# Performance work log

Measured on AMD Instinct MI355X. Metric: run time of the kernel, lower is better.

The kernel has to match this reference:

```python
import jax, jax.numpy as jnp
import numpy as np

HEADS = 8
HEAD_DIM = 32
DIM = 256        # embed_dim; inner_dim = HEADS*HEAD_DIM = 256
DEPTH = 2
MLP_DIM = 1024
GRID_H, GRID_W = 64, 64
CELL_DIM = 15    # pe(0) + in(3) + out(3) + hidden(9)
PE_IN = 3        # cell_pe_patch_dim + cell_in_patch_dim
UPDATE_DIM = 12  # cell_out(3) + hidden(9)
BATCH = 8


def layer_norm(x, g, b, eps=1e-5):
    m = jnp.mean(x, axis=-1, keepdims=True)
    v = jnp.var(x, axis=-1, keepdims=True)
    return (x - m) * jax.lax.rsqrt(v + eps) * g + b


def vit_positional_encoding(n, dim):
    pos = jnp.arange(n, dtype=jnp.float32)[:, None]
    div = jnp.exp(jnp.arange(0, dim, 2, dtype=jnp.float32) * (-np.log(10000.0) / dim))
    pe = jnp.zeros((n, dim), dtype=jnp.float32)
    pe = pe.at[:, 0::2].set(jnp.sin(pos * div)).at[:, 1::2].set(jnp.cos(pos * div))
    return pe[None]  # [1, n, dim]


def localize(x, H, W):
    # x: [b, heads, n, d] with n = H*W. Gather circular 3x3 neighbourhood per position
    # (equivalent to circular pad + one-hot conv in the torch LocalizeAttention).
    b, nh, n, d = x.shape
    y = x.reshape(b, nh, H, W, d)
    neigh = [jnp.roll(y, (1 - ki, 1 - kj), axis=(2, 3)) for ki in range(3) for kj in range(3)]
    return jnp.stack(neigh, axis=4).reshape(b, nh, n, 9, d)  # [b, h, n, 9, d]


def setup_inputs() -> dict:
    key = jax.random.key(0)
    ks = jax.random.split(key, 20)
    d = {}
    d['cells'] = jax.random.normal(ks[0], (BATCH, CELL_DIM, GRID_H, GRID_W), dtype=jnp.float32)
    s = 0.02
    d['We'] = jax.random.normal(ks[1], (CELL_DIM, DIM), jnp.float32) * s
    d['be'] = jnp.zeros((DIM,), jnp.float32)
    d['ln1_g'] = jnp.ones((DEPTH, DIM), jnp.float32)
    d['ln1_b'] = jnp.zeros((DEPTH, DIM), jnp.float32)
    d['Wqkv'] = jax.random.normal(ks[2], (DEPTH, DIM, 3 * HEADS * HEAD_DIM), jnp.float32) * s
    d['Wo'] = jax.random.normal(ks[3], (DEPTH, HEADS * HEAD_DIM, DIM), jnp.float32) * s
    d['bo'] = jnp.zeros((DEPTH, DIM), jnp.float32)
    d['ln2_g'] = jnp.ones((DEPTH, DIM), jnp.float32)
    d['ln2_b'] = jnp.zeros((DEPTH, DIM), jnp.float32)
    d['W1'] = jax.random.normal(ks[4], (DEPTH, DIM, MLP_DIM), jnp.float32) * s
    d['b1'] = jnp.zeros((DEPTH, MLP_DIM), jnp.float32)
    d['W2'] = jax.random.normal(ks[5], (DEPTH, MLP_DIM, DIM), jnp.float32) * s
    d['b2'] = jnp.zeros((DEPTH, DIM), jnp.float32)
    d['lnh_g'] = jnp.ones((DIM,), jnp.float32)
    d['lnh_b'] = jnp.zeros((DIM,), jnp.float32)
    # NOTE: torch zero-inits mlp_head; we use small random weights so the output is nontrivial.
    d['Wh'] = jax.random.normal(ks[6], (DIM, UPDATE_DIM), jnp.float32) * s
    d['bh'] = jnp.zeros((UPDATE_DIM,), jnp.float32)
    return d


def reference(cells, We, be, ln1_g, ln1_b, Wqkv, Wo, bo, ln2_g, ln2_b,
              W1, b1, W2, b2, lnh_g, lnh_b, Wh, bh):
    b, c, H, W = cells.shape
    n = H * W
    x = cells.reshape(b, c, n).transpose(0, 2, 1)           # b n c
    x = x @ We + be                                         # cell_to_embedding
    x = x + vit_positional_encoding(n, x.shape[-1])
    scale = HEAD_DIM ** -0.5
    for l in range(DEPTH):
        y = layer_norm(x, ln1_g[l], ln1_b[l])
        qkv = y @ Wqkv[l]                                   # b n 3*inner
        q, k, v = jnp.split(qkv, 3, axis=-1)
        split_heads = lambda t: t.reshape(b, n, HEADS, HEAD_DIM).transpose(0, 2, 1, 3)
        q, k, v = split_heads(q), split_heads(k), split_heads(v)  # b h n d
        kl = localize(k, H, W)                              # b h n 9 d
        vl = localize(v, H, W)
        dots = jnp.einsum('bhnd,bhnkd->bhnk', q, kl) * scale
        attn = jax.nn.softmax(dots, axis=-1)
        out = jnp.einsum('bhnk,bhnkd->bhnd', attn, vl)
        out = out.transpose(0, 2, 1, 3).reshape(b, n, HEADS * HEAD_DIM)
        x = out @ Wo[l] + bo[l] + x                         # attention + residual
        y = layer_norm(x, ln2_g[l], ln2_b[l])
        y = jax.nn.gelu(y @ W1[l] + b1[l], approximate=False) @ W2[l] + b2[l]
        x = x + y                                           # ffn + residual
    upd = layer_norm(x, lnh_g, lnh_b) @ Wh + bh             # b n UPDATE_DIM
    upd = upd.transpose(0, 2, 1).reshape(b, UPDATE_DIM, H, W)
    # update_rate = 1.0 -> deterministic branch: cells[:, PE_IN:] + update
    updated = cells[:, PE_IN:] + upd
    return jnp.concatenate([cells[:, :PE_IN], updated], axis=1)
```

## Files before the change

### kernel.cpp

```cpp
#include <hip/hip_runtime.h>
#include <hip/hip_bf16.h>
#include <math.h>

#define HEADS 8
#define HEAD_DIM 32
#define DIM 256
#define MLP_DIM 1024
#define NTOK 4096
#define BATCH 8
#define M_TOK (BATCH*NTOK)
#define CELL_DIM 15
#define PE_IN 3
#define UPD 12
#define HME ((size_t)M_TOK*32)

typedef __attribute__((ext_vector_type(8))) short bf16x8;
typedef __attribute__((ext_vector_type(4))) float f32x4;

static __device__ __forceinline__ float bf2f(unsigned short u) {
    return __uint_as_float(((unsigned int)u) << 16);
}
static __device__ __forceinline__ unsigned short f2bf(float f) {
    __hip_bfloat16 h = __float2bfloat16(f);
    union { __hip_bfloat16 h; unsigned short u; } cv; cv.h = h; return cv.u;
}
static __device__ __forceinline__ void gload_lds16(const unsigned short* g, unsigned short* l) {
    __builtin_amdgcn_global_load_lds(
        (const __attribute__((address_space(1))) void*)g,
        (__attribute__((address_space(3))) void*)l, 16, 0, 0);
}
static __device__ __forceinline__ float gelu_fast(float v) {
    return v / (1.f + __expf(-1.59576912f * (v + 0.044715f * v * v * v)));
}

__global__ __launch_bounds__(256) void k_embed(const float* __restrict__ cells,
        const float* __restrict__ We, const float* __restrict__ be,
        const float* __restrict__ g, const float* __restrict__ bln,
        unsigned short* __restrict__ x, unsigned short* __restrict__ y) {
    __shared__ float red[8];
    int tok = blockIdx.x;
    int d = threadIdx.x;
    int b = tok >> 12, n = tok & 4095;
    const float* cb = cells + (size_t)b * CELL_DIM * NTOK + n;
    float acc = 0.f;
#pragma unroll
    for (int c = 0; c < CELL_DIM; ++c)
        acc += cb[c * NTOK] * We[c * DIM + d];
    int i = d >> 1;
    float freq = __expf(-0.03597789f * (float)(2 * i));
    float ph = (float)n * freq;
    float pe = (d & 1) ? __cosf(ph) : __sinf(ph);
    float v = acc + be[d] + pe;
    x[(size_t)tok * DIM + d] = f2bf(v);
    float s = v, ss = v * v;
#pragma unroll
    for (int off = 32; off; off >>= 1) { s += __shfl_xor(s, off); ss += __shfl_xor(ss, off); }
    int wave = d >> 6, lane = d & 63;
    if (lane == 0) { red[wave] = s; red[4 + wave] = ss; }
    __syncthreads();
    float stot = red[0] + red[1] + red[2] + red[3];
    float sstot = red[4] + red[5] + red[6] + red[7];
    float mean = stot * (1.f / DIM);
    float rstd = rsqrtf(sstot * (1.f / DIM) - mean * mean + 1e-5f);
    y[(size_t)tok * DIM + d] = f2bf((v - mean) * rstd * g[d] + bln[d]);
}

__global__ __launch_bounds__(256) void k_prep(const float* __restrict__ Wqkv,
        const float* __restrict__ Wo, const float* __restrict__ W1,
        const float* __restrict__ W2, const float* __restrict__ Wh,
        unsigned short* __restrict__ wT) {
    int seg = blockIdx.y;
    int idx = blockIdx.x * 256 + threadIdx.x;
    if (seg == 8) {
        if (idx >= 16 * 256) return;
        int u = idx >> 8, k = idx & 255;
        wT[1572864 + idx] = (u < UPD) ? f2bf(Wh[(size_t)k * UPD + u]) : (unsigned short)0;
        return;
    }
    int l = seg >> 2, mat = seg & 3;
    const float* src; int kwSh, Nw; size_t ooff;
    switch (mat) {
        case 0: src = Wqkv + (size_t)l * 196608; kwSh = 8;  Nw = 768;  ooff = (size_t)l * 786432 + 0;      break;
        case 1: src = Wo   + (size_t)l * 65536;  kwSh = 8;  Nw = 256;  ooff = (size_t)l * 786432 + 196608; break;
        case 2: src = W1   + (size_t)l * 262144; kwSh = 8;  Nw = 1024; ooff = (size_t)l * 786432 + 262144; break;
        default:src = W2   + (size_t)l * 262144; kwSh = 10; Nw = 256;  ooff = (size_t)l * 786432 + 524288; break;
    }
    int Kw = 1 << kwSh;
    if (idx >= Kw * Nw) return;
    int n = idx >> kwSh, k = idx & (Kw - 1);
    wT[ooff + idx] = f2bf(src[(size_t)k * Nw + n]);
}

template<int EPI, int KT>
__global__ __launch_bounds__(512, 4) void k_mgemm(const unsigned short* __restrict__ A,
        const unsigned short* __restrict__ BT, const float* __restrict__ bias,
        void* __restrict__ Cout, int M, int N, int NT) {
    __shared__ unsigned short As[4][128 * 32];
    __shared__ unsigned short Bs[4][128 * 32];
    int bid = blockIdx.x;
    int cpx = gridDim.x >> 3;
    int sb = (bid & 7) * cpx + (bid >> 3);
    int mt = sb / NT, nt = sb - mt * NT;
    int m0 = mt * 128, n0 = nt * 128;
    int t = threadIdx.x;
    int lane = t & 63, w = t >> 6;
    int wm = (w >> 2) * 64, wn = (w & 3) * 32;
    f32x4 acc[4][2] = {};
    int srow = t >> 2;
    int cg = (t & 3) ^ ((srow >> 1) & 3);
    const unsigned short* aBase = A  + (size_t)(m0 + srow) * KT + cg * 8;
    const unsigned short* bBase = BT + (size_t)(n0 + srow) * KT + cg * 8;
    int fr = lane & 15, kb8 = lane >> 4;

    auto stage = [&](int buf, int k0) {
        gload_lds16(aBase + k0, &As[0][0] + buf * 4096 + t * 8);
        gload_lds16(bBase + k0, &Bs[0][0] + buf * 4096 + t * 8);
    };
    auto compute = [&](int buf) {
        const unsigned short* a = &As[0][0] + buf * 4096;
        const unsigned short* b = &Bs[0][0] + buf * 4096;
        bf16x8 af[4], bfv[2];
#pragma unroll
        for (int i = 0; i < 4; ++i) {
            int r_ = wm + i * 16 + fr;
            af[i] = *(const bf16x8*)&a[r_ * 32 + ((kb8 ^ ((r_ >> 1) & 3)) << 3)];
        }
#pragma unroll
        for (int j = 0; j < 2; ++j) {
            int r_ = wn + j * 16 + fr;
            bfv[j] = *(const bf16x8*)&b[r_ * 32 + ((kb8 ^ ((r_ >> 1) & 3)) << 3)];
        }
        __builtin_amdgcn_s_setprio(1);
#pragma unroll
        for (int i = 0; i < 4; ++i)
#pragma unroll
            for (int j = 0; j < 2; ++j)
                acc[i][j] = __builtin_amdgcn_mfma_f32_16x16x32_bf16(bfv[j], af[i], acc[i][j], 0, 0, 0);
        __builtin_amdgcn_s_setprio(0);
    };

    constexpr int NK = KT >> 5;
    stage(0, 0);
    stage(1, 32);
    stage(2, 64);
    asm volatile("s_waitcnt vmcnt(4)" ::: "memory");
    __builtin_amdgcn_s_barrier();
    __builtin_amdgcn_sched_barrier(0);
#pragma unroll
    for (int k = 0; k < NK - 1; ++k) {
        if (k + 3 < NK) stage((k + 3) & 3, (k + 3) * 32);
        compute(k & 3);
        __builtin_amdgcn_sched_barrier(0);
        if (k + 3 < NK)      asm volatile("s_waitcnt vmcnt(4)" ::: "memory");
        else if (k + 2 < NK) asm volatile("s_waitcnt vmcnt(2)" ::: "memory");
        else                 asm volatile("s_waitcnt vmcnt(0)" ::: "memory");
        __builtin_amdgcn_s_barrier();
        __builtin_amdgcn_sched_barrier(0);
    }
    compute((NK - 1) & 3);

    int mcol = lane & 15, nq = (lane >> 4) * 4;
#pragma unroll
    for (int i = 0; i < 4; ++i) {
        int m = m0 + wm + i * 16 + mcol;
#pragma unroll
        for (int j = 0; j < 2; ++j) {
            int ng = n0 + wn + j * 16 + nq;
            if (EPI == 3) {
                int type = ng >> 8, rem = ng & 255;
                ushort4 pk;
                pk.x = f2bf(acc[i][j][0]); pk.y = f2bf(acc[i][j][1]);
                pk.z = f2bf(acc[i][j][2]); pk.w = f2bf(acc[i][j][3]);
                *(ushort4*)((unsigned short*)Cout +
                    (size_t)(type * 8 + (rem >> 5)) * HME + (size_t)m * 32 + (rem & 31)) = pk;
            } else {
                float4 b4 = *(const float4*)&bias[ng];
                ushort4 pk;
                pk.x = f2bf(gelu_fast(acc[i][j][0] + b4.x));
                pk.y = f2bf(gelu_fast(acc[i][j][1] + b4.y));
                pk.z = f2bf(gelu_fast(acc[i][j][2] + b4.z));
                pk.w = f2bf(gelu_fast(acc[i][j][3] + b4.w));
                *(ushort4*)((unsigned short*)Cout + (size_t)m * N + ng) = pk;
            }
        }
    }
}

template<int ALAYOUT>
__global__ __launch_bounds__(512, 4) void k_mgemm_ln(const unsigned short* __restrict__ A,
        const unsigned short* __restrict__ BT, const float* __restrict__ bias,
        const float* __restrict__ g, const float* __restrict__ bln,
        unsigned short* __restrict__ x, unsigned short* __restrict__ y, int K) {
    __shared__ unsigned short As[3][64 * 32];
    __shared__ unsigned short Bs[3][256 * 32];
    float* sred = (float*)&As[0][0];
    float* ssred = sred + 512;
    float* msr = ssred + 512;
    int t = threadIdx.x;
    int lane = t & 63, w = t >> 6;
    int wn = w * 32;
    int m0 = blockIdx.x * 64;
    int mloc = lane & 15, nq = (lane >> 4) * 4;

    ushort4 xres[4][2];
#pragma unroll
    for (int i = 0; i < 4; ++i) {
        int gm = m0 + i * 16 + mloc;
#pragma unroll
        for (int j = 0; j < 2; ++j)
            xres[i][j] = *(const ushort4*)&x[(size_t)gm * DIM + wn + j * 16 + nq];
    }
    __builtin_amdgcn_sched_barrier(0);

    f32x4 acc[4][2] = {};
    int rB0 = t >> 2, cgB0 = (t & 3) ^ ((rB0 >> 1) & 3);
    int c1 = t + 512;
    int rB1 = c1 >> 2, cgB1 = (c1 & 3) ^ ((rB1 >> 1) & 3);
    int tA = t & 255;
    int rA = tA >> 2, cgA = (tA & 3) ^ ((rA >> 1) & 3);
    const unsigned short* aBase = (ALAYOUT == 0)
        ? A + (size_t)(m0 + rA) * K + cgA * 8
        : A + (size_t)(m0 + rA) * 32 + cgA * 8;
    const unsigned short* b0Base = BT + (size_t)rB0 * K + cgB0 * 8;
    const unsigned short* b1Base = BT + (size_t)rB1 * K + cgB1 * 8;
    int fr = lane & 15, kb8 = lane >> 4;

    auto stage = [&](int buf, int k0) {
        unsigned short* as_ = &As[0][0] + buf * 2048;
        unsigned short* bs_ = &Bs[0][0] + buf * 8192;
        gload_lds16(b0Base + k0, bs_ + t * 8);
        gload_lds16(b1Base + k0, bs_ + 4096 + t * 8);
        if (t < 256) {
            const unsigned short* aSrc = (ALAYOUT == 0) ? aBase + k0 : aBase + (size_t)(k0 >> 5) * HME;
            gload_lds16(aSrc, as_ + tA * 8);
        } else {
            gload_lds16(b0Base + k0, bs_ + t * 8);
        }
    };
    auto compute = [&](int buf) {
        const unsigned short* as_ = &As[0][0] + buf * 2048;
        const unsigned short* bs_ = &Bs[0][0] + buf * 8192;
        bf16x8 af[4], bfv[2];
#pragma unroll
        for (int i = 0; i < 4; ++i) {
            int r_ = i * 16 + fr;
            af[i] = *(const bf16x8*)&as_[r_ * 32 + ((kb8 ^ ((r_ >> 1) & 3)) << 3)];
        }
#pragma unroll
        for (int j = 0; j < 2; ++j) {
            int rl = wn + j * 16 + fr;
            bfv[j] = *(const bf16x8*)&bs_[rl * 32 + ((kb8 ^ ((rl >> 1) & 3)) << 3)];
        }
        __builtin_amdgcn_s_setprio(1);
#pragma unroll
        for (int i = 0; i < 4; ++i)
#pragma unroll
            for (int j = 0; j < 2; ++j)
                acc[i][j] = __builtin_amdgcn_mfma_f32_16x16x32_bf16(bfv[j], af[i], acc[i][j], 0, 0, 0);
        __builtin_amdgcn_s_setprio(0);
    };

    int nk = K >> 5;
    stage(0, 0);
    stage(1, 32);
    asm volatile("s_waitcnt vmcnt(3)" ::: "memory");
    __builtin_amdgcn_s_barrier();
    __builtin_amdgcn_sched_barrier(0);
    int cur = 0;
    for (int k = 0; k < nk - 1; ++k) {
        int pre = k + 2;
        if (pre < nk) {
            int preBuf = cur + 2; if (preBuf >= 3) preBuf -= 3;
            stage(preBuf, pre * 32);
        }
        compute(cur);
        __builtin_amdgcn_sched_barrier(0);
        if (pre < nk) asm volatile("s_waitcnt vmcnt(3)" ::: "memory");
        else          asm volatile("s_waitcnt vmcnt(0)" ::: "memory");
        __builtin_amdgcn_s_barrier();
        __builtin_amdgcn_sched_barrier(0);
        ++cur; if (cur >= 3) cur -= 3;
    }
    compute(cur);
    __syncthreads();

#pragma unroll
    for (int i = 0; i < 4; ++i) {
        float s = 0.f, ss = 0.f;
#pragma unroll
        for (int j = 0; j < 2; ++j) {
            int nb = wn + j * 16 + nq;
            float4 b4 = *(const float4*)&bias[nb];
            acc[i][j][0] += b4.x + bf2f(xres[i][j].x);
            acc[i][j][1] += b4.y + bf2f(xres[i][j].y);
            acc[i][j][2] += b4.z + bf2f(xres[i][j].z);
            acc[i][j][3] += b4.w + bf2f(xres[i][j].w);
#pragma unroll
            for (int r = 0; r < 4; ++r) { float v = acc[i][j][r]; s += v; ss += v * v; }
        }
        s += __shfl_xor(s, 16); ss += __shfl_xor(ss, 16);
        s += __shfl_xor(s, 32); ss += __shfl_xor(ss, 32);
        if (lane < 16) {
            int row = i * 16 + lane;
            sred[row * 8 + w] = s;
            ssred[row * 8 + w] = ss;
        }
    }
    __syncthreads();
    if (t < 64) {
        float s = 0.f, ss = 0.f;
#pragma unroll
        for (int q = 0; q < 8; ++q) { s += sred[t * 8 + q]; ss += ssred[t * 8 + q]; }
        float mean = s * (1.f / DIM);
        float var = ss * (1.f / DIM) - mean * mean;
        msr[t * 2] = mean;
        msr[t * 2 + 1] = rsqrtf(var + 1e-5f);
    }
    __syncthreads();
#pragma unroll
    for (int i = 0; i < 4; ++i) {
        int row = i * 16 + mloc;
        int gm = m0 + row;
        float mean = msr[row * 2], rstd = msr[row * 2 + 1];
#pragma unroll
        for (int j = 0; j < 2; ++j) {
            int nb = wn + j * 16 + nq;
            float4 gv4 = *(const float4*)&g[nb];
            float4 bb4 = *(const float4*)&bln[nb];
            ushort4 xo;
            xo.x = f2bf(acc[i][j][0]); xo.y = f2bf(acc[i][j][1]);
            xo.z = f2bf(acc[i][j][2]); xo.w = f2bf(acc[i][j][3]);
            *(ushort4*)&x[(size_t)gm * DIM + nb] = xo;
            ushort4 yv;
            yv.x = f2bf((acc[i][j][0] - mean) * rstd * gv4.x + bb4.x);
            yv.y = f2bf((acc[i][j][1] - mean) * rstd * gv4.y + bb4.y);
            yv.z = f2bf((acc[i][j][2] - mean) * rstd * gv4.z + bb4.z);
            yv.w = f2bf((acc[i][j][3] - mean) * rstd * gv4.w + bb4.w);
            *(ushort4*)&y[(size_t)gm * DIM + nb] = yv;
        }
    }
}

__global__ __launch_bounds__(256) void k_attn(const unsigned short* __restrict__ qkvH,
        unsigned short* __restrict__ attnH) {
    int t = threadIdx.x;
    int h = t >> 5, tl = t & 31;
    int tok = blockIdx.x * 32 + tl;
    int b = tok >> 12, n = tok & 4095;
    int r = n >> 6, c = n & 63;

    float q[32];
    {
        const uint4* u = (const uint4*)(qkvH + (size_t)h * HME + (size_t)tok * 32);
#pragma unroll
        for (int i = 0; i < 4; ++i) {
            uint4 x4 = u[i];
            unsigned wv[4] = {x4.x, x4.y, x4.z, x4.w};
#pragma unroll
            for (int wj = 0; wj < 4; ++wj) {
                q[i * 8 + wj * 2]     = __uint_as_float(wv[wj] << 16);
                q[i * 8 + wj * 2 + 1] = __uint_as_float(wv[wj] & 0xffff0000u);
            }
        }
    }
    int nts[9];
    float dots[9];
    const unsigned short* kbase = qkvH + (size_t)(8 + h) * HME;
#pragma unroll
    for (int ki = 0; ki < 3; ++ki)
#pragma unroll
        for (int kj = 0; kj < 3; ++kj) {
            int rr = (r + ki - 1) & 63, cc = (c + kj - 1) & 63;
            int nt = (b << 12) + (rr << 6) + cc;
            nts[ki * 3 + kj] = nt;
            const uint4* u = (const uint4*)(kbase + (size_t)nt * 32);
            float acc = 0.f;
#pragma unroll
            for (int i = 0; i < 4; ++i) {
                uint4 x4 = u[i];
                unsigned wv[4] = {x4.x, x4.y, x4.z, x4.w};
#pragma unroll
                for (int wj = 0; wj < 4; ++wj) {
                    acc += __uint_as_float(wv[wj] << 16)        * q[i * 8 + wj * 2];
                    acc += __uint_as_float(wv[wj] & 0xffff0000u) * q[i * 8 + wj * 2 + 1];
                }
            }
            dots[ki * 3 + kj] = acc * 0.17677669529f;
        }
    float m = dots[0];
#pragma unroll
    for (int j = 1; j < 9; ++j) m = fmaxf(m, dots[j]);
    float sum = 0.f;
#pragma unroll
    for (int j = 0; j < 9; ++j) { dots[j] = __expf(dots[j] - m); sum += dots[j]; }
    float inv = 1.f / sum;
    float o[32] = {};
    const unsigned short* vbase = qkvH + (size_t)(16 + h) * HME;
#pragma unroll
    for (int j = 0; j < 9; ++j) {
        float wgt = dots[j] * inv;
        const uint4* u = (const uint4*)(vbase + (size_t)nts[j] * 32);
#pragma unroll
        for (int i = 0; i < 4; ++i) {
            uint4 x4 = u[i];
            unsigned wv[4] = {x4.x, x4.y, x4.z, x4.w};
#pragma unroll
            for (int wj = 0; wj < 4; ++wj) {
                o[i * 8 + wj * 2]     += wgt * __uint_as_float(wv[wj] << 16);
                o[i * 8 + wj * 2 + 1] += wgt * __uint_as_float(wv[wj] & 0xffff0000u);
            }
        }
    }
    uint4 st[4];
    unsigned* sw = (unsigned*)st;
#pragma unroll
    for (int i = 0; i < 16; ++i)
        sw[i] = (unsigned)f2bf(o[2 * i]) | ((unsigned)f2bf(o[2 * i + 1]) << 16);
    uint4* od = (uint4*)(attnH + (size_t)h * HME + (size_t)tok * 32);
#pragma unroll
    for (int i = 0; i < 4; ++i) od[i] = st[i];
}

__global__ __launch_bounds__(256) void k_headgemv(const unsigned short* __restrict__ y,
        const unsigned short* __restrict__ WhT, float* __restrict__ Cg) {
    int t = threadIdx.x, lane = t & 63, w = t >> 6;
    int m0 = blockIdx.x * 64 + w * 16;
    int fr = lane & 15, kb = (lane >> 4) * 8;
    f32x4 acc = {};
    const unsigned short* aRow = y + (size_t)(m0 + fr) * DIM + kb;
    const unsigned short* bRow = WhT + (size_t)fr * DIM + kb;
#pragma unroll
    for (int k0 = 0; k0 < DIM; k0 += 32) {
        bf16x8 a = *(const bf16x8*)(aRow + k0);
        bf16x8 bfr = *(const bf16x8*)(bRow + k0);
        acc = __builtin_amdgcn_mfma_f32_16x16x32_bf16(a, bfr, acc, 0, 0, 0);
    }
    int col = lane & 15, rowq = (lane >> 4) * 4;
#pragma unroll
    for (int r = 0; r < 4; ++r)
        Cg[(size_t)(m0 + rowq + r) * 16 + col] = acc[r];
}

__global__ __launch_bounds__(256) void k_assemble(const float* __restrict__ cells,
        const float* __restrict__ Cg, const float* __restrict__ bh,
        float* __restrict__ outp) {
    int idx = blockIdx.x * 256 + threadIdx.x;
    int total = BATCH * CELL_DIM * (NTOK / 4);
    if (idx >= total) return;
    int n4 = idx & 1023;
    int c = (idx >> 10) % CELL_DIM;
    int b = idx / (CELL_DIM * 1024);
    size_t ci = ((size_t)b * CELL_DIM + c) * NTOK + n4 * 4;
    float4 o = *(const float4*)(cells + ci);
    if (c >= PE_IN) {
        int u = c - PE_IN;
        float bias = bh[u];
        size_t tok = (size_t)b * NTOK + n4 * 4;
        o.x += Cg[(tok + 0) * 16 + u] + bias;
        o.y += Cg[(tok + 1) * 16 + u] + bias;
        o.z += Cg[(tok + 2) * 16 + u] + bias;
        o.w += Cg[(tok + 3) * 16 + u] + bias;
    }
    *(float4*)(outp + ci) = o;
}

extern "C" void kernel_launch(void* const* d_in, const int* in_sizes, int n_in,
                              void* d_out, int out_size, void* d_ws, size_t ws_size,
                              hipStream_t stream) {
    const float* cells = (const float*)d_in[0];
    const float* We    = (const float*)d_in[1];
    const float* be    = (const float*)d_in[2];
    const float* ln1_g = (const float*)d_in[3];
    const float* ln1_b = (const float*)d_in[4];
    const float* Wqkv  = (const float*)d_in[5];
    const float* Wo    = (const float*)d_in[6];
    const float* bo    = (const float*)d_in[7];
    const float* ln2_g = (const float*)d_in[8];
    const float* ln2_b = (const float*)d_in[9];
    const float* W1    = (const float*)d_in[10];
    const float* b1    = (const float*)d_in[11];
    const float* W2    = (const float*)d_in[12];
    const float* b2    = (const float*)d_in[13];
    const float* lnh_g = (const float*)d_in[14];
    const float* lnh_b = (const float*)d_in[15];
    const float* Wh    = (const float*)d_in[16];
    const float* bh    = (const float*)d_in[17];
    float* outp = (float*)d_out;

    char* ws = (char*)d_ws;
    unsigned short* x = (unsigned short*)ws;
    unsigned short* y = (unsigned short*)(ws + 33554432);
    unsigned short* scratch = (unsigned short*)(ws + 50331648);
    unsigned short* wT = (unsigned short*)(ws + 117440512);
    unsigned short* qkvH  = scratch;
    unsigned short* attnH = scratch + 24 * HME;
    unsigned short* hidden = scratch;
    float* Cg = (float*)scratch;

    k_prep<<<dim3(1024, 9), 256, 0, stream>>>(Wqkv, Wo, W1, W2, Wh, wT);
    k_embed<<<M_TOK, 256, 0, stream>>>(cells, We, be, ln1_g, ln1_b, x, y);
    for (int l = 0; l < 2; ++l) {
        const unsigned short* wL = wT + (size_t)l * 786432;
        const float* gN = (l == 0) ? ln1_g + DIM : lnh_g;
        const float* bN = (l == 0) ? ln1_b + DIM : lnh_b;
        k_mgemm<3, 256><<<1536, 512, 0, stream>>>(
            y, wL + 0, nullptr, qkvH, M_TOK, 768, 6);
        k_attn<<<M_TOK / 32, 256, 0, stream>>>(qkvH, attnH);
        k_mgemm_ln<1><<<M_TOK / 64, 512, 0, stream>>>(
            attnH, wL + 196608, bo + l * DIM, ln2_g + l * DIM, ln2_b + l * DIM, x, y, DIM);
        k_mgemm<1, 256><<<2048, 512, 0, stream>>>(
            y, wL + 262144, b1 + l * MLP_DIM, hidden, M_TOK, MLP_DIM, 8);
        k_mgemm_ln<0><<<M_TOK / 64, 512, 0, stream>>>(
            hidden, wL + 524288, b2 + l * DIM, gN, bN, x, y, MLP_DIM);
    }
    k_headgemv<<<M_TOK / 64, 256, 0, stream>>>(y, wT + 1572864, Cg);
    k_assemble<<<(BATCH * CELL_DIM * (NTOK / 4) + 255) / 256, 256, 0, stream>>>(cells, Cg, bh, outp);
}
```

Baseline: 368.2 us.

## Make QKV and FFN1 GEMMs persistent over four M-tiles with continuous pipeline

```diff
diff --git a/kernel.cpp b/kernel.cpp
--- a/kernel.cpp
+++ b/kernel.cpp
@@ -91,7 +91,7 @@
     wT[ooff + idx] = f2bf(src[(size_t)k * Nw + n]);
 }
 
-template<int EPI, int KT>
+template<int EPI, int KT, int T>
 __global__ __launch_bounds__(512, 4) void k_mgemm(const unsigned short* __restrict__ A,
         const unsigned short* __restrict__ BT, const float* __restrict__ bias,
         void* __restrict__ Cout, int M, int N, int NT) {
@@ -100,21 +100,26 @@
     int bid = blockIdx.x;
     int cpx = gridDim.x >> 3;
     int sb = (bid & 7) * cpx + (bid >> 3);
-    int mt = sb / NT, nt = sb - mt * NT;
-    int m0 = mt * 128, n0 = nt * 128;
+    int mg = sb / NT, nt = sb - mg * NT;
+    int m0g = mg * (128 * T), n0 = nt * 128;
     int t = threadIdx.x;
     int lane = t & 63, w = t >> 6;
     int wm = (w >> 2) * 64, wn = (w & 3) * 32;
     f32x4 acc[4][2] = {};
     int srow = t >> 2;
     int cg = (t & 3) ^ ((srow >> 1) & 3);
-    const unsigned short* aBase = A  + (size_t)(m0 + srow) * KT + cg * 8;
+    const unsigned short* aBase = A  + (size_t)(m0g + srow) * KT + cg * 8;
     const unsigned short* bBase = BT + (size_t)(n0 + srow) * KT + cg * 8;
     int fr = lane & 15, kb8 = lane >> 4;
-
-    auto stage = [&](int buf, int k0) {
-        gload_lds16(aBase + k0, &As[0][0] + buf * 4096 + t * 8);
-        gload_lds16(bBase + k0, &Bs[0][0] + buf * 4096 + t * 8);
+    constexpr int NK = KT >> 5;
+    constexpr int S = NK * T;
+
+    auto stageU = [&](int u) {
+        int buf = u & 3;
+        int tau = u >> 3, kk = u & 7;
+        gload_lds16(aBase + (size_t)tau * 128 * KT + kk * 32,
+                    &As[0][0] + buf * 4096 + t * 8);
+        gload_lds16(bBase + kk * 32, &Bs[0][0] + buf * 4096 + t * 8);
     };
     auto compute = [&](int buf) {
         const unsigned short* a = &As[0][0] + buf * 4096;
@@ -138,50 +143,67 @@
                 acc[i][j] = __builtin_amdgcn_mfma_f32_16x16x32_bf16(bfv[j], af[i], acc[i][j], 0, 0, 0);
         __builtin_amdgcn_s_setprio(0);
     };
-
-    constexpr int NK = KT >> 5;
-    stage(0, 0);
-    stage(1, 32);
-    stage(2, 64);
+    int mcol = lane & 15, nq = (lane >> 4) * 4;
+    auto epilogue = [&](int tau) {
+        int mBase = m0g + tau * 128;
+#pragma unroll
+        for (int i = 0; i < 4; ++i) {
+            int m = mBase + wm + i * 16 + mcol;
+#pragma unroll
+            for (int j = 0; j < 2; ++j) {
+                int ng = n0 + wn + j * 16 + nq;
+                if (EPI == 3) {
+                    int type = ng >> 8, rem = ng & 255;
+                    ushort4 pk;
+                    pk.x = f2bf(acc[i][j][0]); pk.y = f2bf(acc[i][j][1]);
+                    pk.z = f2bf(acc[i][j][2]); pk.w = f2bf(acc[i][j][3]);
+                    *(ushort4*)((unsigned short*)Cout +
+                        (size_t)(type * 8 + (rem >> 5)) * HME + (size_t)m * 32 + (rem & 31)) = pk;
+                } else {
+                    float4 b4 = *(const float4*)&bias[ng];
+                    ushort4 pk;
+                    pk.x = f2bf(gelu_fast(acc[i][j][0] + b4.x));
+                    pk.y = f2bf(gelu_fast(acc[i][j][1] + b4.y));
+                    pk.z = f2bf(gelu_fast(acc[i][j][2] + b4.z));
+                    pk.w = f2bf(gelu_fast(acc[i][j][3] + b4.w));
+                    *(ushort4*)((unsigned short*)Cout + (size_t)m * N + ng) = pk;
+                }
+            }
+        }
+    };
+
+    stageU(0); stageU(1); stageU(2);
     asm volatile("s_waitcnt vmcnt(4)" ::: "memory");
     __builtin_amdgcn_s_barrier();
     __builtin_amdgcn_sched_barrier(0);
-#pragma unroll
-    for (int k = 0; k < NK - 1; ++k) {
-        if (k + 3 < NK) stage((k + 3) & 3, (k + 3) * 32);
-        compute(k & 3);
-        __builtin_amdgcn_sched_barrier(0);
-        if (k + 3 < NK)      asm volatile("s_waitcnt vmcnt(4)" ::: "memory");
-        else if (k + 2 < NK) asm volatile("s_waitcnt vmcnt(2)" ::: "memory");
-        else                 asm volatile("s_waitcnt vmcnt(0)" ::: "memory");
-        __builtin_amdgcn_s_barrier();
-        __builtin_amdgcn_sched_barrier(0);
-    }
-    compute((NK - 1) & 3);
-
-    int mcol = lane & 15, nq = (lane >> 4) * 4;
-#pragma unroll
-    for (int i = 0; i < 4; ++i) {
-        int m = m0 + wm + i * 16 + mcol;
-#pragma unroll
-        for (int j = 0; j < 2; ++j) {
-            int ng = n0 + wn + j * 16 + nq;
-            if (EPI == 3) {
-                int type = ng >> 8, rem = ng & 255;
-                ushort4 pk;
-                pk.x = f2bf(acc[i][j][0]); pk.y = f2bf(acc[i][j][1]);
-                pk.z = f2bf(acc[i][j][2]); pk.w = f2bf(acc[i][j][3]);
-                *(ushort4*)((unsigned short*)Cout +
-                    (size_t)(type * 8 + (rem >> 5)) * HME + (size_t)m * 32 + (rem & 31)) = pk;
+    for (int tau = 0; tau < T; ++tau) {
+#pragma unroll
+        for (int kk = 0; kk < NK; ++kk) {
+            int s = tau * NK + kk;
+            if (s + 3 < S) stageU(s + 3);
+            compute(s & 3);
+            if (kk == NK - 1) {
+                epilogue(tau);
+                if (tau < T - 1) {
+#pragma unroll
+                    for (int i = 0; i < 4; ++i)
+#pragma unroll
+                        for (int j = 0; j < 2; ++j) acc[i][j] = (f32x4){0.f, 0.f, 0.f, 0.f};
+                }
+            }
+            __builtin_amdgcn_sched_barrier(0);
+            if (s == S - 1) break;
+            bool slack = (kk == NK - 1) || (tau > 0 && kk <= 1);
+            if (s + 3 < S) {
+                if (slack) asm volatile("s_waitcnt vmcnt(12)" ::: "memory");
+                else       asm volatile("s_waitcnt vmcnt(4)"  ::: "memory");
+            } else if (s == S - 3) {
+                asm volatile("s_waitcnt vmcnt(2)" ::: "memory");
             } else {
-                float4 b4 = *(const float4*)&bias[ng];
-                ushort4 pk;
-                pk.x = f2bf(gelu_fast(acc[i][j][0] + b4.x));
-                pk.y = f2bf(gelu_fast(acc[i][j][1] + b4.y));
-                pk.z = f2bf(gelu_fast(acc[i][j][2] + b4.z));
-                pk.w = f2bf(gelu_fast(acc[i][j][3] + b4.w));
-                *(ushort4*)((unsigned short*)Cout + (size_t)m * N + ng) = pk;
+                asm volatile("s_waitcnt vmcnt(0)" ::: "memory");
             }
+            __builtin_amdgcn_s_barrier();
+            __builtin_amdgcn_sched_barrier(0);
         }
     }
 }
@@ -503,12 +525,12 @@
         const unsigned short* wL = wT + (size_t)l * 786432;
         const float* gN = (l == 0) ? ln1_g + DIM : lnh_g;
         const float* bN = (l == 0) ? ln1_b + DIM : lnh_b;
-        k_mgemm<3, 256><<<1536, 512, 0, stream>>>(
+        k_mgemm<3, 256, 4><<<384, 512, 0, stream>>>(
             y, wL + 0, nullptr, qkvH, M_TOK, 768, 6);
         k_attn<<<M_TOK / 32, 256, 0, stream>>>(qkvH, attnH);
         k_mgemm_ln<1><<<M_TOK / 64, 512, 0, stream>>>(
             attnH, wL + 196608, bo + l * DIM, ln2_g + l * DIM, ln2_b + l * DIM, x, y, DIM);
-        k_mgemm<1, 256><<<2048, 512, 0, stream>>>(
+        k_mgemm<1, 256, 4><<<512, 512, 0, stream>>>(
             y, wL + 262144, b1 + l * MLP_DIM, hidden, M_TOK, MLP_DIM, 8);
         k_mgemm_ln<0><<<M_TOK / 64, 512, 0, stream>>>(
             hidden, wL + 524288, b2 + l * DIM, gN, bN, x, y, MLP_DIM);
```

After: 375.2 us. No clear change (+1.9%).

## Tile local attention over 16x16 spatial patches with K/V halo in LDS

Applied to the files above, without the earlier changes.

```diff
diff --git a/kernel.cpp b/kernel.cpp
--- a/kernel.cpp
+++ b/kernel.cpp
@@ -343,12 +343,16 @@
 
 __global__ __launch_bounds__(256) void k_attn(const unsigned short* __restrict__ qkvH,
         unsigned short* __restrict__ attnH) {
+    __shared__ unsigned short Ks[324 * 40];
+    __shared__ unsigned short Vs[324 * 40];
+    int bid = blockIdx.x;
+    int b = bid >> 7, h = (bid >> 4) & 7, pr = (bid >> 2) & 3, pc = bid & 3;
     int t = threadIdx.x;
-    int h = t >> 5, tl = t & 31;
-    int tok = blockIdx.x * 32 + tl;
-    int b = tok >> 12, n = tok & 4095;
-    int r = n >> 6, c = n & 63;
-
+    int ty = t >> 4, tx = t & 15;
+    const unsigned short* kplane = qkvH + (size_t)(8 + h) * HME;
+    const unsigned short* vplane = qkvH + (size_t)(16 + h) * HME;
+
+    int tok = (b << 12) + ((pr * 16 + ty) << 6) + (pc * 16 + tx);
     float q[32];
     {
         const uint4* u = (const uint4*)(qkvH + (size_t)h * HME + (size_t)tok * 32);
@@ -363,25 +367,37 @@
             }
         }
     }
-    int nts[9];
+    for (int s = t; s < 324; s += 256) {
+        int sr = s / 18, sc = s - sr * 18;
+        int gr = (pr * 16 + sr - 1) & 63, gc = (pc * 16 + sc - 1) & 63;
+        size_t nt = ((size_t)b << 12) + (gr << 6) + gc;
+        const uint4* ksrc = (const uint4*)(kplane + nt * 32);
+        const uint4* vsrc = (const uint4*)(vplane + nt * 32);
+#pragma unroll
+        for (int i = 0; i < 4; ++i) {
+            *(uint4*)&Ks[s * 40 + i * 8] = ksrc[i];
+            *(uint4*)&Vs[s * 40 + i * 8] = vsrc[i];
+        }
+    }
+    __syncthreads();
+
     float dots[9];
-    const unsigned short* kbase = qkvH + (size_t)(8 + h) * HME;
+    int slots[9];
 #pragma unroll
     for (int ki = 0; ki < 3; ++ki)
 #pragma unroll
         for (int kj = 0; kj < 3; ++kj) {
-            int rr = (r + ki - 1) & 63, cc = (c + kj - 1) & 63;
-            int nt = (b << 12) + (rr << 6) + cc;
-            nts[ki * 3 + kj] = nt;
-            const uint4* u = (const uint4*)(kbase + (size_t)nt * 32);
+            int slot = (ty + ki) * 18 + (tx + kj);
+            slots[ki * 3 + kj] = slot;
+            const unsigned short* kp = &Ks[slot * 40];
             float acc = 0.f;
 #pragma unroll
             for (int i = 0; i < 4; ++i) {
-                uint4 x4 = u[i];
+                uint4 x4 = *(const uint4*)(kp + i * 8);
                 unsigned wv[4] = {x4.x, x4.y, x4.z, x4.w};
 #pragma unroll
                 for (int wj = 0; wj < 4; ++wj) {
-                    acc += __uint_as_float(wv[wj] << 16)        * q[i * 8 + wj * 2];
+                    acc += __uint_as_float(wv[wj] << 16)         * q[i * 8 + wj * 2];
                     acc += __uint_as_float(wv[wj] & 0xffff0000u) * q[i * 8 + wj * 2 + 1];
                 }
             }
@@ -395,14 +411,13 @@
     for (int j = 0; j < 9; ++j) { dots[j] = __expf(dots[j] - m); sum += dots[j]; }
     float inv = 1.f / sum;
     float o[32] = {};
-    const unsigned short* vbase = qkvH + (size_t)(16 + h) * HME;
 #pragma unroll
     for (int j = 0; j < 9; ++j) {
         float wgt = dots[j] * inv;
-        const uint4* u = (const uint4*)(vbase + (size_t)nts[j] * 32);
+        const unsigned short* vp = &Vs[slots[j] * 40];
 #pragma unroll
         for (int i = 0; i < 4; ++i) {
-            uint4 x4 = u[i];
+            uint4 x4 = *(const uint4*)(vp + i * 8);
             unsigned wv[4] = {x4.x, x4.y, x4.z, x4.w};
 #pragma unroll
             for (int wj = 0; wj < 4; ++wj) {
@@ -505,7 +520,7 @@
         const float* bN = (l == 0) ? ln1_b + DIM : lnh_b;
         k_mgemm<3, 256><<<1536, 512, 0, stream>>>(
             y, wL + 0, nullptr, qkvH, M_TOK, 768, 6);
-        k_attn<<<M_TOK / 32, 256, 0, stream>>>(qkvH, attnH);
+        k_attn<<<1024, 256, 0, stream>>>(qkvH, attnH);
         k_mgemm_ln<1><<<M_TOK / 64, 512, 0, stream>>>(
             attnH, wL + 196608, bo + l * DIM, ln2_g + l * DIM, ln2_b + l * DIM, x, y, DIM);
         k_mgemm<1, 256><<<2048, 512, 0, stream>>>(
```

Result: faster. 331.5 us (-10.0%).
